# Kernel optimization log

Measured on AMD Instinct MI355X. Metric: run time of the kernel, lower is better.

## Reference

```python
import jax, jax.numpy as jnp
import numpy as np
from jax import lax

KS = 3       # kernel_size
PAD = 1      # padding
STRIDE = 1
DIL = 2      # dilation (scales adaptive offsets)
N = KS * KS
DN = ('NCHW', 'OIHW', 'NCHW')


def _conv(x, w, stride, padding):
    return lax.conv_general_dilated(x, w, (stride, stride),
                                    [(padding, padding), (padding, padding)],
                                    dimension_numbers=DN)


def _deform_forward(x, w_p, b_p, w_m, w_ad, w_conv):
    B, C, H, W = x.shape
    offset = _conv(x, w_p, STRIDE, 1) + b_p[None, :, None, None]      # (B,2N,H,W)
    ad_base = 1.0 - jax.nn.sigmoid(_conv(x, w_ad, STRIDE, 1))         # (B,KS,H,W)
    ad = jnp.tile(ad_base, (1, 2 * KS, 1, 1)) * DIL                   # (B,2N,H,W)
    ad_m = jnp.tile((ad_base - 0.5) * 2.0, (1, KS, 1, 1)) * DIL       # (B,N,H,W)
    m = jax.nn.sigmoid(_conv(x, w_m, STRIDE, 1))                      # (B,N,H,W)

    # kernel relative offsets p_n: (1,2N,1,1)
    r = jnp.arange(-(KS - 1) // 2, (KS - 1) // 2 + 1, dtype=x.dtype)
    pnx, pny = jnp.meshgrid(r, r, indexing='ij')
    p_n = jnp.concatenate([pnx.ravel(), pny.ravel()])[None, :, None, None]
    # base sampling coords p_0: (1,2N,H,W), offset by 1 to match zero padding
    ix = jnp.arange(1, H * STRIDE + 1, STRIDE, dtype=x.dtype)
    iy = jnp.arange(1, W * STRIDE + 1, STRIDE, dtype=x.dtype)
    p0x, p0y = jnp.meshgrid(ix, iy, indexing='ij')
    p_0 = jnp.concatenate([jnp.broadcast_to(p0x, (1, N, H, W)),
                           jnp.broadcast_to(p0y, (1, N, H, W))], axis=1)

    p = p_0 + p_n + offset + ad * p_n                                  # (B,2N,H,W)
    p = p.transpose(0, 2, 3, 1)                                        # (B,H,W,2N)

    xp = jnp.pad(x, ((0, 0), (0, 0), (PAD, PAD), (PAD, PAD)))         # (B,C,Hp,Wp)
    Hp, Wp = H + 2 * PAD, W + 2 * PAD

    q_lt = jnp.floor(p)
    q_rb = q_lt + 1.0

    def clampxy(q):
        return jnp.concatenate([jnp.clip(q[..., :N], 0, Hp - 1),
                                jnp.clip(q[..., N:], 0, Wp - 1)], -1).astype(jnp.int32)

    q_lt = clampxy(q_lt)
    q_rb = clampxy(q_rb)
    q_lb = jnp.concatenate([q_lt[..., :N], q_rb[..., N:]], -1)
    q_rt = jnp.concatenate([q_rb[..., :N], q_lt[..., N:]], -1)

    # out-of-range mask (detached); snap those points to floor, then clamp
    mask = jnp.concatenate([
        (p[..., :N] < PAD) | (p[..., :N] > Hp - 1 - PAD),
        (p[..., N:] < PAD) | (p[..., N:] > Wp - 1 - PAD)], -1).astype(p.dtype)
    mask = lax.stop_gradient(mask)
    p = p * (1 - mask) + jnp.floor(p) * mask
    p = jnp.concatenate([jnp.clip(p[..., :N], 0, Hp - 1),
                         jnp.clip(p[..., N:], 0, Wp - 1)], -1)

    def g(q, sx, sy):  # bilinear weights
        qx = q[..., :N].astype(p.dtype)
        qy = q[..., N:].astype(p.dtype)
        return (1 + sx * (qx - p[..., :N])) * (1 + sy * (qy - p[..., N:]))

    g_lt = g(q_lt, 1, 1)
    g_rb = g(q_rb, -1, -1)
    g_lb = g(q_lb, 1, -1)
    g_rt = g(q_rt, -1, 1)

    x_flat = xp.reshape(B, C, Hp * Wp)
    L = H * W * N

    def gather(q):
        idx = (q[..., :N] * Wp + q[..., N:]).reshape(B, 1, L)
        idx = jnp.broadcast_to(idx, (B, C, L))
        return jnp.take_along_axis(x_flat, idx, axis=2).reshape(B, C, H, W, N)

    x_off = (g_lt[:, None] * gather(q_lt) + g_rb[:, None] * gather(q_rb)
             + g_lb[:, None] * gather(q_lb) + g_rt[:, None] * gather(q_rt))

    # modulation scaled by adaptive term
    mm = (m * ad_m).transpose(0, 2, 3, 1)[:, None]                     # (B,1,H,W,N)
    x_off = x_off * mm

    # (B,C,H,W,ks*ks) -> (B,C,H*ks,W*ks)
    x_off = x_off.reshape(B, C, H, W, KS, KS).transpose(0, 1, 2, 4, 3, 5)
    x_off = x_off.reshape(B, C, H * KS, W * KS)
    return _conv(x_off, w_conv, KS, 0)                                 # (B,Cout,H,W)


def setup_inputs() -> dict:
    key = jax.random.key(0)
    ks = jax.random.split(key, 6)
    C_in, C_out = 64, 64
    x = jax.random.normal(ks[0], (2, C_in, 128, 128), jnp.float32)
    w_p = jax.random.normal(ks[1], (2 * N, C_in, 3, 3), jnp.float32) * 0.01
    b_p = jax.random.normal(ks[2], (2 * N,), jnp.float32) * 0.01
    w_m = jax.random.normal(ks[3], (N, C_in, 3, 3), jnp.float32) * 0.05
    w_ad = jax.random.normal(ks[4], (KS, C_in, 3, 3), jnp.float32) * 0.05
    w_conv = jax.random.normal(ks[5], (C_out, C_in, KS, KS), jnp.float32) / np.sqrt(C_in * N).astype(np.float32)
    return {"x": x, "w_p": w_p, "b_p": b_p, "w_m": w_m, "w_ad": w_ad, "w_conv": w_conv}


def reference(x, w_p, b_p, w_m, w_ad, w_conv):
    return _deform_forward(x, w_p, b_p, w_m, w_ad, w_conv)
```

## Files before the change

kernel.cpp:

```cpp
#include <hip/hip_runtime.h>
#include <hip/hip_fp16.h>
#include <math.h>

#define H 128
#define W 128
#define BATCH 2

typedef short short8 __attribute__((ext_vector_type(8)));
typedef float f32x4 __attribute__((ext_vector_type(4)));
typedef float f32x16 __attribute__((ext_vector_type(16)));

#define BPLANE 1081600
#define PLANE  2163200
#define XS_M   PLANE
#define WC_OFF (2 * PLANE)
#define WM_OFF (WC_OFF + 36864)
#define WM_PLANE 18432
#define META_OFF (WM_OFF + 2 * WM_PLANE)

__device__ __forceinline__ unsigned f2bf_u(float f) {
    union { float f; unsigned u; } v; v.f = f;
    return (v.u + 0x7FFFu + ((v.u >> 16) & 1u)) >> 16;
}
__device__ __forceinline__ float bfbits2f(unsigned lo16) {
    union { unsigned u; float f; } v; v.u = lo16 << 16;
    return v.f;
}
__device__ __forceinline__ float bfs2f(short s) {
    union { unsigned u; float f; } v; v.u = ((unsigned)(unsigned short)s) << 16;
    return v.f;
}
__device__ __forceinline__ void split2(float v, unsigned& h, unsigned& m) {
    h = f2bf_u(v);
    float r1 = v - bfbits2f(h);
    m = f2bf_u(r1);
}

__global__ __launch_bounds__(256) void prep_kernel(
    const float* __restrict__ x, const float* __restrict__ w_p,
    const float* __restrict__ w_m, const float* __restrict__ w_ad,
    const float* __restrict__ w_conv, unsigned short* __restrict__ ws)
{
    const int blk = blockIdx.x, t = threadIdx.x;
    if (blk < 520) {
        int code = blk >> 1, chalf = blk & 1;
        int b = code / 130, hrow = code % 130;
        size_t rb = ((size_t)b * 16900 + hrow * 130) * 32;
        unsigned* uh = (unsigned*)ws + rb;
        unsigned* um = (unsigned*)(ws + XS_M) + rb;
        if (hrow == 0 || hrow == 129) {
            for (int f = t + chalf * 2080; f < 2080 + chalf * 2080; f += 256) {
                uh[f] = 0; um[f] = 0;
            }
            return;
        }
        __shared__ float s[64 * 65];
        int h = hrow - 1;
        for (int f = t; f < 64 * 64; f += 256) {
            int ci = f >> 6, w = f & 63;
            s[ci * 65 + w] = x[((b * 64 + ci) * 128 + h) * 128 + chalf * 64 + w];
        }
        __syncthreads();
        for (int f = t; f < 2048; f += 256) {
            int w = f >> 5, cip = f & 31;
            unsigned h0, m0, h1, m1;
            split2(s[(2 * cip) * 65 + w], h0, m0);
            split2(s[(2 * cip + 1) * 65 + w], h1, m1);
            int o = (chalf * 64 + w + 1) * 32 + cip;
            uh[o] = h0 | (h1 << 16);
            um[o] = m0 | (m1 << 16);
        }
        if (chalf == 0) { if (t < 32) { uh[t] = 0; um[t] = 0; } }
        else           { if (t < 32) { int o = 129 * 32 + t; uh[o] = 0; um[o] = 0; } }
    } else if (blk < 556) {
        int q = (blk - 520) * 256 + t;
        int e = q * 4;
        int j = e & 15, co = (e >> 4) & 63, kk = e >> 10;
        int klin = kk * 16 + j;
        int n = klin >> 6, ci = klin & 63;
        const float* src = w_conv + co * 576 + n;
        ushort4 r;
        r.x = (unsigned short)f2bf_u(src[(ci + 0) * 9]);
        r.y = (unsigned short)f2bf_u(src[(ci + 1) * 9]);
        r.z = (unsigned short)f2bf_u(src[(ci + 2) * 9]);
        r.w = (unsigned short)f2bf_u(src[(ci + 3) * 9]);
        *(ushort4*)(ws + WC_OFF + e) = r;
    } else {
        int q = (blk - 556) * 256 + t;
        int oc = q / 576, k = q % 576;
        int s = k >> 6, ci = k & 63;
        float v = 0.f;
        if (oc < 18)      v = w_p[oc * 576 + ci * 9 + s];
        else if (oc < 21) v = w_ad[(oc - 18) * 576 + ci * 9 + s];
        else if (oc < 30) v = w_m[(oc - 21) * 576 + ci * 9 + s];
        unsigned hh, mm; split2(v, hh, mm);
        ws[WM_OFF + q] = (unsigned short)hh;
        ws[WM_OFF + WM_PLANE + q] = (unsigned short)mm;
    }
}

__global__ __launch_bounds__(512, 2) void meta_kernel(
    const float* __restrict__ b_p, const unsigned short* __restrict__ wsu,
    float* __restrict__ meta)
{
    __shared__ __align__(16) unsigned short s_w[64 * 584];
    const int t = threadIdx.x;
    const int d = blockIdx.x;
    const int l = (d & 7) * 32 + (d >> 3);
    const int b = l >> 7, i = l & 127;

    #pragma unroll
    for (int it = 0; it < 9; ++it) {
        int chunk = it * 512 + t;
        int r = chunk / 72, c8 = chunk % 72;
        *(short8*)(s_w + r * 584 + c8 * 8) =
            *(const short8*)(wsu + WM_OFF + chunk * 8);
    }
    __syncthreads();

    const int wv = t >> 6, lane = t & 63, lr = lane & 15, lg = lane >> 4;
    const int px = wv * 16 + lr;
    const unsigned short* xsb = wsu + (size_t)b * BPLANE;

    f32x4 aA0 = {0,0,0,0}, aB0 = {0,0,0,0}, aA1 = {0,0,0,0}, aB1 = {0,0,0,0};
    #pragma unroll
    for (int kk = 0; kk < 18; ++kk) {
        const int s = kk >> 1;
        const unsigned short* bp = xsb + ((i + s / 3) * 130 + (px + s % 3)) * 64
                                   + ((kk & 1) << 5) + lg * 8;
        short8 bh = *(const short8*)(bp);
        short8 bm = *(const short8*)(bp + XS_M);
        const unsigned short* w0 = s_w + lr * 584 + kk * 32 + lg * 8;
        short8 ah0 = *(const short8*)(w0);
        short8 am0 = *(const short8*)(w0 + 32 * 584);
        const unsigned short* w1 = w0 + 16 * 584;
        short8 ah1 = *(const short8*)(w1);
        short8 am1 = *(const short8*)(w1 + 32 * 584);
        aA0 = __builtin_amdgcn_mfma_f32_16x16x32_bf16(ah0, bh, aA0, 0, 0, 0);
        aB0 = __builtin_amdgcn_mfma_f32_16x16x32_bf16(ah0, bm, aB0, 0, 0, 0);
        aA0 = __builtin_amdgcn_mfma_f32_16x16x32_bf16(am0, bh, aA0, 0, 0, 0);
        aA1 = __builtin_amdgcn_mfma_f32_16x16x32_bf16(ah1, bh, aA1, 0, 0, 0);
        aB1 = __builtin_amdgcn_mfma_f32_16x16x32_bf16(ah1, bm, aB1, 0, 0, 0);
        aA1 = __builtin_amdgcn_mfma_f32_16x16x32_bf16(am1, bh, aA1, 0, 0, 0);
    }

    float* mb = meta + (((size_t)b * 128 + i) * 128 + px) * 32;
    {
        const float4 bq = *(const float4*)(b_p + lg * 4);
        f32x4 o0;
        o0[0] = aA0[0] + aB0[0] + bq.x;
        o0[1] = aA0[1] + aB0[1] + bq.y;
        o0[2] = aA0[2] + aB0[2] + bq.z;
        o0[3] = aA0[3] + aB0[3] + bq.w;
        *(f32x4*)(mb + lg * 4) = o0;
    }
    {
        f32x4 o1;
        #pragma unroll
        for (int r = 0; r < 4; ++r) {
            int oc = 16 + lg * 4 + r;
            float v = aA1[r] + aB1[r];
            if (oc < 18)      v += b_p[oc];
            else if (oc < 21) v = 1.f - 1.f / (1.f + expf(-v));
            else              v = 1.f / (1.f + expf(-v));
            o1[r] = v;
        }
        *(f32x4*)(mb + 16 + lg * 4) = o1;
    }
}

__global__ __launch_bounds__(512, 8) void deform_kernel(
    const unsigned short* __restrict__ wsu, const float* __restrict__ meta,
    float* __restrict__ out)
{
    __shared__ __align__(16) char smem[40832];
    unsigned short* s_valb = (unsigned short*)smem;
    __half2* s_gh = (__half2*)(smem + 37376);
    int* s_idxp = (int*)(smem + 39680);

    const int t = threadIdx.x;
    const int d = blockIdx.x;
    const int l = (d & 7) * 128 + (d >> 3);
    const int jb = l & 3, i = (l >> 2) & 127, b = l >> 9;
    const int j0 = jb * 32;

    if (t < 288) {
        int pix = t / 9, n = t % 9;
        int ki = n / 3, kj = n % 3;
        const float* mrow = meta + (((size_t)b * 128 + i) * 128 + j0 + pix) * 32;
        float adb  = mrow[18 + kj];
        float offx = mrow[n];
        float offy = mrow[9 + n];
        float msig = mrow[21 + n];
        float pnx = (float)(ki - 1), pny = (float)(kj - 1);
        float pxc = (float)(i + 1)        + pnx + offx + 2.f * adb * pnx;
        float pyc = (float)(j0 + pix + 1) + pny + offy + 2.f * adb * pny;

        float flx = floorf(pxc), fly = floorf(pyc);
        int ix0 = (int)fminf(fmaxf(flx,       0.f), 129.f);
        int ix1 = (int)fminf(fmaxf(flx + 1.f, 0.f), 129.f);
        int iy0 = (int)fminf(fmaxf(fly,       0.f), 129.f);
        int iy1 = (int)fminf(fmaxf(fly + 1.f, 0.f), 129.f);

        float ptx = (pxc < 1.f || pxc > 128.f) ? flx : pxc;
        float pty = (pyc < 1.f || pyc > 128.f) ? fly : pyc;
        ptx = fminf(fmaxf(ptx, 0.f), 129.f);
        pty = fminf(fmaxf(pty, 0.f), 129.f);

        float wxl = 1.f + (float)ix0 - ptx;
        float wxr = 1.f - ((float)ix1 - ptx);
        float wyl = 1.f + (float)iy0 - pty;
        float wyr = 1.f - ((float)iy1 - pty);

        float mm = msig * (adb - 0.5f) * 4.f;

        s_gh[t * 2 + 0] = __floats2half2_rn(wxl * wyl * mm, wxr * wyr * mm);
        s_gh[t * 2 + 1] = __floats2half2_rn(wxl * wyr * mm, wxr * wyl * mm);
        s_idxp[t] = ix0 | (ix1 << 8) | (iy0 << 16) | (iy1 << 24);
    }
    __syncthreads();

    const unsigned short* xsb = wsu + (size_t)b * BPLANE;
    #define GATHER(TASK) do {                                                     \
        int task = (TASK);                                                        \
        int n = task >> 8, pix = (task >> 3) & 31, cig = task & 7;                \
        int pk = s_idxp[pix * 9 + n];                                             \
        int ix0 = pk & 255, ix1 = (pk >> 8) & 255;                                \
        int iy0 = (pk >> 16) & 255, iy1 = (pk >> 24) & 255;                       \
        const unsigned short* base = xsb + cig * 8;                               \
        short8 v00 = *(const short8*)(base + (ix0 * 130 + iy0) * 64);             \
        short8 v11 = *(const short8*)(base + (ix1 * 130 + iy1) * 64);             \
        short8 v01 = *(const short8*)(base + (ix0 * 130 + iy1) * 64);             \
        short8 v10 = *(const short8*)(base + (ix1 * 130 + iy0) * 64);             \
        float2 g01 = __half22float2(s_gh[(pix * 9 + n) * 2 + 0]);                 \
        float2 g23 = __half22float2(s_gh[(pix * 9 + n) * 2 + 1]);                 \
        unsigned po[4];                                                           \
        _Pragma("unroll")                                                         \
        for (int jp = 0; jp < 4; ++jp) {                                          \
            float e0 = g01.x * bfs2f(v00[2 * jp])     + g01.y * bfs2f(v11[2 * jp])\
                     + g23.x * bfs2f(v01[2 * jp])     + g23.y * bfs2f(v10[2 * jp]);\
            float e1 = g01.x * bfs2f(v00[2 * jp + 1]) + g01.y * bfs2f(v11[2 * jp + 1])\
                     + g23.x * bfs2f(v01[2 * jp + 1]) + g23.y * bfs2f(v10[2 * jp + 1]);\
            po[jp] = f2bf_u(e0) | (f2bf_u(e1) << 16);                             \
        }                                                                         \
        *(uint4*)(s_valb + pix * 584 + n * 64 + cig * 8)                          \
            = make_uint4(po[0], po[1], po[2], po[3]);                             \
    } while (0)

    #pragma unroll
    for (int it = 0; it < 4; ++it) GATHER(t + it * 512);
    if (t < 256) GATHER(t + 2048);
    #undef GATHER
    __syncthreads();

    {
        const int w = t >> 6, lane = t & 63;
        const int ch = w & 1, kq = w >> 1;
        const int colA = lane & 31, hi = lane >> 5;
        const unsigned short* wa = wsu + WC_OFF + ((kq * 9) * 64 + ch * 32 + colA) * 16 + hi * 8;
        const unsigned short* vb = s_valb + colA * 584 + (kq * 9) * 16 + hi * 8;
        f32x16 acc = {0,0,0,0,0,0,0,0,0,0,0,0,0,0,0,0};
        #pragma unroll
        for (int s = 0; s < 9; ++s) {
            short8 a   = *(const short8*)(wa + s * 1024);
            short8 bfr = *(const short8*)(vb + s * 16);
            acc = __builtin_amdgcn_mfma_f32_32x32x16_bf16(a, bfr, acc, 0, 0, 0);
        }
        __syncthreads();
        float* sp = (float*)smem;
        #pragma unroll
        for (int r = 0; r < 16; ++r)
            sp[(w * 16 + r) * 65 + lane] = acc[r];
        __syncthreads();
        int ch2 = t >> 8, e = t & 255;
        int lane2 = e & 63, rq = e >> 6;
        #pragma unroll
        for (int q = 0; q < 4; ++q) {
            int reg = rq * 4 + q;
            float v = sp[((0 + ch2) * 16 + reg) * 65 + lane2]
                    + sp[((2 + ch2) * 16 + reg) * 65 + lane2]
                    + sp[((4 + ch2) * 16 + reg) * 65 + lane2]
                    + sp[((6 + ch2) * 16 + reg) * 65 + lane2];
            int col = lane2 & 31;
            int row = (reg & 3) + 8 * (reg >> 2) + 4 * (lane2 >> 5);
            int co = ch2 * 32 + row;
            out[(((size_t)b * 64 + co) * 128 + i) * 128 + j0 + col] = v;
        }
    }
}

extern "C" void kernel_launch(void* const* d_in, const int* in_sizes, int n_in,
                              void* d_out, int out_size, void* d_ws, size_t ws_size,
                              hipStream_t stream) {
    const float* x      = (const float*)d_in[0];
    const float* w_p    = (const float*)d_in[1];
    const float* b_p    = (const float*)d_in[2];
    const float* w_m    = (const float*)d_in[3];
    const float* w_ad   = (const float*)d_in[4];
    const float* w_conv = (const float*)d_in[5];
    float* outp = (float*)d_out;
    unsigned short* ws = (unsigned short*)d_ws;
    float* meta_f = (float*)(ws + META_OFF);

    prep_kernel<<<628, 256, 0, stream>>>(x, w_p, w_m, w_ad, w_conv, ws);
    meta_kernel<<<256, 512, 0, stream>>>(b_p, ws, meta_f);
    deform_kernel<<<1024, 512, 0, stream>>>(ws, meta_f, outp);
}
```

Measured before the change: 36.95 us.

## Fuse offset/mask convolution into deform kernel, removing meta kernel and buffer

After: 39.71 us. +7.5%, slower.

```diff
diff --git a/kernel.cpp b/kernel.cpp
--- a/kernel.cpp
+++ b/kernel.cpp
@@ -16,7 +16,6 @@
 #define WC_OFF (2 * PLANE)
 #define WM_OFF (WC_OFF + 36864)
 #define WM_PLANE 18432
-#define META_OFF (WM_OFF + 2 * WM_PLANE)
 
 __device__ __forceinline__ unsigned f2bf_u(float f) {
     union { float f; unsigned u; } v; v.f = f;
@@ -87,8 +86,9 @@
         *(ushort4*)(ws + WC_OFF + e) = r;
     } else {
         int q = (blk - 556) * 256 + t;
-        int oc = q / 576, k = q % 576;
-        int s = k >> 6, ci = k & 63;
+        int oc = (q >> 4) & 31, j = q & 15, kk = q >> 9;
+        int klin = kk * 16 + j;
+        int s = klin >> 6, ci = klin & 63;
         float v = 0.f;
         if (oc < 18)      v = w_p[oc * 576 + ci * 9 + s];
         else if (oc < 21) v = w_ad[(oc - 18) * 576 + ci * 9 + s];
@@ -99,95 +99,74 @@
     }
 }
 
-__global__ __launch_bounds__(512, 2) void meta_kernel(
+__global__ __launch_bounds__(512, 6) void deform_kernel(
     const float* __restrict__ b_p, const unsigned short* __restrict__ wsu,
-    float* __restrict__ meta)
-{
-    __shared__ __align__(16) unsigned short s_w[64 * 584];
-    const int t = threadIdx.x;
-    const int d = blockIdx.x;
-    const int l = (d & 7) * 32 + (d >> 3);
-    const int b = l >> 7, i = l & 127;
-
-    #pragma unroll
-    for (int it = 0; it < 9; ++it) {
-        int chunk = it * 512 + t;
-        int r = chunk / 72, c8 = chunk % 72;
-        *(short8*)(s_w + r * 584 + c8 * 8) =
-            *(const short8*)(wsu + WM_OFF + chunk * 8);
-    }
-    __syncthreads();
-
-    const int wv = t >> 6, lane = t & 63, lr = lane & 15, lg = lane >> 4;
-    const int px = wv * 16 + lr;
-    const unsigned short* xsb = wsu + (size_t)b * BPLANE;
-
-    f32x4 aA0 = {0,0,0,0}, aB0 = {0,0,0,0}, aA1 = {0,0,0,0}, aB1 = {0,0,0,0};
-    #pragma unroll
-    for (int kk = 0; kk < 18; ++kk) {
-        const int s = kk >> 1;
-        const unsigned short* bp = xsb + ((i + s / 3) * 130 + (px + s % 3)) * 64
-                                   + ((kk & 1) << 5) + lg * 8;
-        short8 bh = *(const short8*)(bp);
-        short8 bm = *(const short8*)(bp + XS_M);
-        const unsigned short* w0 = s_w + lr * 584 + kk * 32 + lg * 8;
-        short8 ah0 = *(const short8*)(w0);
-        short8 am0 = *(const short8*)(w0 + 32 * 584);
-        const unsigned short* w1 = w0 + 16 * 584;
-        short8 ah1 = *(const short8*)(w1);
-        short8 am1 = *(const short8*)(w1 + 32 * 584);
-        aA0 = __builtin_amdgcn_mfma_f32_16x16x32_bf16(ah0, bh, aA0, 0, 0, 0);
-        aB0 = __builtin_amdgcn_mfma_f32_16x16x32_bf16(ah0, bm, aB0, 0, 0, 0);
-        aA0 = __builtin_amdgcn_mfma_f32_16x16x32_bf16(am0, bh, aA0, 0, 0, 0);
-        aA1 = __builtin_amdgcn_mfma_f32_16x16x32_bf16(ah1, bh, aA1, 0, 0, 0);
-        aB1 = __builtin_amdgcn_mfma_f32_16x16x32_bf16(ah1, bm, aB1, 0, 0, 0);
-        aA1 = __builtin_amdgcn_mfma_f32_16x16x32_bf16(am1, bh, aA1, 0, 0, 0);
-    }
-
-    float* mb = meta + (((size_t)b * 128 + i) * 128 + px) * 32;
-    {
-        const float4 bq = *(const float4*)(b_p + lg * 4);
-        f32x4 o0;
-        o0[0] = aA0[0] + aB0[0] + bq.x;
-        o0[1] = aA0[1] + aB0[1] + bq.y;
-        o0[2] = aA0[2] + aB0[2] + bq.z;
-        o0[3] = aA0[3] + aB0[3] + bq.w;
-        *(f32x4*)(mb + lg * 4) = o0;
-    }
-    {
-        f32x4 o1;
-        #pragma unroll
-        for (int r = 0; r < 4; ++r) {
-            int oc = 16 + lg * 4 + r;
-            float v = aA1[r] + aB1[r];
-            if (oc < 18)      v += b_p[oc];
-            else if (oc < 21) v = 1.f - 1.f / (1.f + expf(-v));
-            else              v = 1.f / (1.f + expf(-v));
-            o1[r] = v;
-        }
-        *(f32x4*)(mb + 16 + lg * 4) = o1;
-    }
-}
-
-__global__ __launch_bounds__(512, 8) void deform_kernel(
-    const unsigned short* __restrict__ wsu, const float* __restrict__ meta,
     float* __restrict__ out)
 {
-    __shared__ __align__(16) char smem[40832];
+    __shared__ __align__(16) char smem[44928];
     unsigned short* s_valb = (unsigned short*)smem;
-    __half2* s_gh = (__half2*)(smem + 37376);
-    int* s_idxp = (int*)(smem + 39680);
+    float* s_part = (float*)smem;
+    float* s_meta = (float*)(smem + 37376);
+    __half2* s_gh = (__half2*)(smem + 41472);
+    int* s_idxp = (int*)(smem + 43776);
 
     const int t = threadIdx.x;
     const int d = blockIdx.x;
     const int l = (d & 7) * 128 + (d >> 3);
     const int jb = l & 3, i = (l >> 2) & 127, b = l >> 9;
     const int j0 = jb * 32;
+    const unsigned short* xsb = wsu + (size_t)b * BPLANE;
+
+    const int w = t >> 6, lane = t & 63;
+    const int colA = lane & 31, hi = lane >> 5;
+
+    {
+        const int kq = w >> 1, sub = w & 1;
+        f32x16 acc = {0,0,0,0,0,0,0,0,0,0,0,0,0,0,0,0};
+        #pragma unroll
+        for (int it9 = 0; it9 < 9; ++it9) {
+            int kk = kq * 9 + it9;
+            int s = kk >> 2;
+            int sr = s / 3, sc = s - sr * 3;
+            const unsigned short* bp = xsb + ((i + sr) * 130 + (j0 + colA + sc)) * 64
+                                       + (kk & 3) * 16 + hi * 8;
+            const unsigned short* ap = wsu + WM_OFF + (kk * 32 + colA) * 16 + hi * 8;
+            short8 ah = *(const short8*)ap;
+            if (sub == 0) {
+                short8 am = *(const short8*)(ap + WM_PLANE);
+                short8 bh = *(const short8*)bp;
+                acc = __builtin_amdgcn_mfma_f32_32x32x16_bf16(ah, bh, acc, 0, 0, 0);
+                acc = __builtin_amdgcn_mfma_f32_32x32x16_bf16(am, bh, acc, 0, 0, 0);
+            } else {
+                short8 bm = *(const short8*)(bp + XS_M);
+                acc = __builtin_amdgcn_mfma_f32_32x32x16_bf16(ah, bm, acc, 0, 0, 0);
+            }
+        }
+        #pragma unroll
+        for (int r = 0; r < 16; ++r)
+            s_part[(w * 16 + r) * 65 + lane] = acc[r];
+    }
+    __syncthreads();
+
+    for (int o = t; o < 960; o += 512) {
+        int oc = o >> 5, px = o & 31;
+        int lane2 = px + ((oc >> 2) & 1) * 32;
+        int reg = (oc & 3) + 4 * (oc >> 3);
+        float v = 0.f;
+        #pragma unroll
+        for (int w2 = 0; w2 < 8; ++w2)
+            v += s_part[(w2 * 16 + reg) * 65 + lane2];
+        if (oc < 18)      v += b_p[oc];
+        else if (oc < 21) v = 1.f - 1.f / (1.f + expf(-v));
+        else              v = 1.f / (1.f + expf(-v));
+        s_meta[px * 32 + oc] = v;
+    }
+    __syncthreads();
 
     if (t < 288) {
         int pix = t / 9, n = t % 9;
         int ki = n / 3, kj = n % 3;
-        const float* mrow = meta + (((size_t)b * 128 + i) * 128 + j0 + pix) * 32;
+        const float* mrow = s_meta + pix * 32;
         float adb  = mrow[18 + kj];
         float offx = mrow[n];
         float offy = mrow[9 + n];
@@ -220,7 +199,6 @@
     }
     __syncthreads();
 
-    const unsigned short* xsb = wsu + (size_t)b * BPLANE;
     #define GATHER(TASK) do {                                                     \
         int task = (TASK);                                                        \
         int n = task >> 8, pix = (task >> 3) & 31, cig = task & 7;                \
@@ -254,9 +232,7 @@
     __syncthreads();
 
     {
-        const int w = t >> 6, lane = t & 63;
         const int ch = w & 1, kq = w >> 1;
-        const int colA = lane & 31, hi = lane >> 5;
         const unsigned short* wa = wsu + WC_OFF + ((kq * 9) * 64 + ch * 32 + colA) * 16 + hi * 8;
         const unsigned short* vb = s_valb + colA * 584 + (kq * 9) * 16 + hi * 8;
         f32x16 acc = {0,0,0,0,0,0,0,0,0,0,0,0,0,0,0,0};
@@ -300,9 +276,7 @@
     const float* w_conv = (const float*)d_in[5];
     float* outp = (float*)d_out;
     unsigned short* ws = (unsigned short*)d_ws;
-    float* meta_f = (float*)(ws + META_OFF);
 
     prep_kernel<<<628, 256, 0, stream>>>(x, w_p, w_m, w_ad, w_conv, ws);
-    meta_kernel<<<256, 512, 0, stream>>>(b_p, ws, meta_f);
-    deform_kernel<<<1024, 512, 0, stream>>>(ws, meta_f, outp);
-}
+    deform_kernel<<<1024, 512, 0, stream>>>(b_p, ws, outp);
+}
```
